# Kernel tuning notes

Measured on AMD Instinct MI355X. Metric: run time of the kernel, lower is better.

## Reference

```python
import jax, jax.numpy as jnp
import numpy as np
import math

B, IN, D, H, DEPTH, E, K = 16384, 128, 512, 8, 3, 8, 2
FF, EH = 4 * D, 256          # ffn width = 4*d_model; expert hidden fixed at 256 in source
EPSILON = 0.1                # forward() default epsilon (exploration mixing)
LN_EPS = 1e-5


def _ln(x, w, b):
    m = x.mean(-1, keepdims=True)
    v = x.var(-1, keepdims=True)  # biased variance, matching nn.LayerNorm
    return (x - m) / jnp.sqrt(v + LN_EPS) * w + b


def setup_inputs() -> dict:
    key = jax.random.key(0)
    ks = jax.random.split(key, 16)
    s = 0.02
    rn = lambda k, shape: jax.random.normal(k, shape, jnp.float32) * s
    return dict(
        x=jax.random.normal(ks[0], (B, IN), jnp.float32),
        embed_w=rn(ks[1], (IN, D)), embed_b=jnp.zeros((D,), jnp.float32),
        ln1_w=jnp.ones((DEPTH, D), jnp.float32), ln1_b=jnp.zeros((DEPTH, D), jnp.float32),
        inproj_w=rn(ks[2], (DEPTH, 3 * D, D)), inproj_b=jnp.zeros((DEPTH, 3 * D), jnp.float32),
        outproj_w=rn(ks[3], (DEPTH, D, D)), outproj_b=jnp.zeros((DEPTH, D), jnp.float32),
        ln2_w=jnp.ones((DEPTH, D), jnp.float32), ln2_b=jnp.zeros((DEPTH, D), jnp.float32),
        ffn_w1=rn(ks[4], (DEPTH, D, FF)), ffn_b1=jnp.zeros((DEPTH, FF), jnp.float32),
        ffn_w2=rn(ks[5], (DEPTH, FF, D)), ffn_b2=jnp.zeros((DEPTH, D), jnp.float32),
        router_w=rn(ks[6], (D, E)), router_b=jnp.zeros((E,), jnp.float32),
        exp_w1=rn(ks[7], (E, D, EH)), exp_b1=jnp.zeros((E, EH), jnp.float32),
        exp_w2=rn(ks[8], (E, EH, D)), exp_b2=jnp.zeros((E, D), jnp.float32),
        head_ln_w=jnp.ones((D,), jnp.float32), head_ln_b=jnp.zeros((D,), jnp.float32),
        head_w=rn(ks[9], (D, 1)), head_b=jnp.zeros((1,), jnp.float32),
    )


def reference(x, embed_w, embed_b, ln1_w, ln1_b, inproj_w, inproj_b,
              outproj_w, outproj_b, ln2_w, ln2_b, ffn_w1, ffn_b1, ffn_w2, ffn_b2,
              router_w, router_b, exp_w1, exp_b1, exp_w2, exp_b2,
              head_ln_w, head_ln_b, head_w, head_b):
    h = x @ embed_w + embed_b                       # [B, D]; unsqueeze(1) -> seq_len == 1
    for l in range(DEPTH):
        g = _ln(h, ln1_w[l], ln1_b[l])
        qkv = g @ inproj_w[l].T + inproj_b[l]       # [B, 3D]
        # seq_len == 1: softmax over the single key is exactly 1, so attn(h,h,h) == out_proj(V)
        v = qkv[:, 2 * D:]
        a = v @ outproj_w[l].T + outproj_b[l]
        h = h + a
        g = _ln(h, ln2_w[l], ln2_b[l])
        h = h + jax.nn.gelu(g @ ffn_w1[l] + ffn_b1[l], approximate=False) @ ffn_w2[l] + ffn_b2[l]
    z = h                                           # squeeze(1)

    # WaggleGate
    logits = z @ router_w + router_b                # [B, E]
    probs = jax.nn.softmax(logits, axis=-1)
    probs = (1.0 - EPSILON) * probs + EPSILON / E
    wts, idx = jax.lax.top_k(probs, K)              # [B, K]
    load = probs.mean(0)
    aux = (load * jnp.log(load * E + 1e-9)).sum() / math.log(E + 1e-9)

    # dense all-expert compute + sparse top-k combine (same math as per-sample dispatch)
    hmid = jax.nn.gelu(jnp.einsum('bd,edh->ebh', z, exp_w1) + exp_b1[:, None, :], approximate=False)
    eo = jnp.einsum('ebh,ehd->ebd', hmid, exp_w2) + exp_b2[:, None, :]   # [E, B, D]
    gate = jnp.zeros((z.shape[0], E), z.dtype).at[
        jnp.arange(z.shape[0])[:, None], idx].add(wts)                    # [B, E]
    moe = jnp.einsum('be,ebd->bd', gate, eo)

    z = z + moe
    logit = (_ln(z, head_ln_w, head_ln_b) @ head_w + head_b)[:, 0]       # [B]
    return logit, aux
```

## Files before the change

kernel.cpp:

```cpp
#include <hip/hip_runtime.h>
#include <hip/hip_bf16.h>

#define B_TOK 16384
#define IN_DIM 128
#define D_DIM 512
#define DEPTH 3
#define NEXP 8
#define FF_DIM 2048
#define EH_DIM 256
#define MAXSLOT 33792
#define MAXTILE 264
#define NHBLK 64

typedef __attribute__((ext_vector_type(8))) __bf16 bf16x8;
typedef __attribute__((ext_vector_type(4))) float f32x4;
typedef __attribute__((ext_vector_type(4))) unsigned short u16x4;
typedef __attribute__((ext_vector_type(8))) unsigned short u16x8;

__device__ __forceinline__ unsigned short f2bf(float f){
    unsigned int u = __float_as_uint(f);
    u += 0x7fffu + ((u >> 16) & 1u);
    return (unsigned short)(u >> 16);
}
__device__ __forceinline__ float bf2f(unsigned short u){
    return __uint_as_float(((unsigned int)u) << 16);
}
__device__ __forceinline__ float geluf(float x){
    return 0.5f * x * (1.0f + erff(x * 0.70710678118654752f));
}
__device__ __forceinline__ void gload_lds16(const void* g, void* l){
    __builtin_amdgcn_global_load_lds((const __attribute__((address_space(1))) unsigned int*)g,
                                     (__attribute__((address_space(3))) unsigned int*)l,
                                     16, 0, 0);
}

__global__ void zero_kernel(int* a, int na, int* b, int nb){
    const int i = blockIdx.x * blockDim.x + threadIdx.x;
    if (i < na) a[i] = 0;
    if (i < nb) b[i] = 0;
}

struct ConvSeg { const float* src; unsigned short* dst; int n4; };
struct ConvArgs { ConvSeg seg[2]; };

__global__ void convert_kernel(ConvArgs a){
    const int stride = gridDim.x * blockDim.x;
    const int tid = blockIdx.x * blockDim.x + threadIdx.x;
    for (int s = 0; s < 2; ++s){
        const f32x4* src = (const f32x4*)a.seg[s].src;
        u16x4* dst = (u16x4*)a.seg[s].dst;
        const int n4 = a.seg[s].n4;
        for (int i = tid; i < n4; i += stride){
            f32x4 v = src[i];
            u16x4 o;
            o[0] = f2bf(v[0]); o[1] = f2bf(v[1]); o[2] = f2bf(v[2]); o[3] = f2bf(v[3]);
            dst[i] = o;
        }
    }
}

struct TSeg { const float* src; unsigned short* dst; int K; int N; int tileStart; };
struct TArgs { TSeg seg[26]; };

__global__ void transpose_kernel(TArgs a){
    __shared__ float t[32][33];
    const int tile = blockIdx.x;
    int s = 0;
    #pragma unroll 1
    while (s < 25 && tile >= a.seg[s+1].tileStart) ++s;
    const TSeg sg = a.seg[s];
    const int local = tile - sg.tileStart;
    const int tilesN = sg.N >> 5;
    const int k0 = (local / tilesN) << 5;
    const int n0 = (local % tilesN) << 5;
    const int tx = threadIdx.x & 31;
    const int ty = threadIdx.x >> 5;
    #pragma unroll
    for (int j = 0; j < 4; ++j)
        t[ty + j*8][tx] = sg.src[(size_t)(k0 + ty + j*8) * sg.N + n0 + tx];
    __syncthreads();
    #pragma unroll
    for (int j = 0; j < 4; ++j){
        const int n = ty + j*8;
        sg.dst[(size_t)(n0 + n) * sg.K + k0 + tx] = f2bf(t[tx][n]);
    }
}

__global__ void foldb_kernel(const float* __restrict__ outproj_w, const float* __restrict__ outproj_b,
                             const float* __restrict__ inproj_b, float* __restrict__ bfold){
    const int l = blockIdx.x, n = threadIdx.x;
    const float* Wo = outproj_w + ((size_t)l*D_DIM + n)*D_DIM;
    const float* bv = inproj_b + l*3*D_DIM + 2*D_DIM;
    float acc = outproj_b[l*D_DIM + n];
    for (int j = 0; j < D_DIM; ++j) acc += Wo[j]*bv[j];
    bfold[l*D_DIM + n] = acc;
}

#define EPI_BF16 0
#define EPI_BF16_GELU 1
#define EPI_F32_BIAS 2
#define EPI_F32_RESID 3

template<int EPI>
__global__ void __launch_bounds__(256, 2)
gemm_bt(const unsigned short* __restrict__ A, const unsigned short* __restrict__ Bt,
        const float* __restrict__ bias, const float* __restrict__ resid,
        void* __restrict__ out, int M, int N, int K)
{
    __shared__ unsigned short sh[16384];
    unsigned short* Al = sh;
    unsigned short* Bl = sh + 8192;
    const int tid  = threadIdx.x;
    const int lane = tid & 63;
    const int wave = tid >> 6;
    const int wm = (wave >> 1) << 6;
    const int wn = (wave & 1) << 6;
    const int bm = blockIdx.y, bn = blockIdx.x;

    f32x4 acc[4][4] = {};

    const unsigned short* Abase = A + (size_t)bm * 128 * K;
    const unsigned short* Bbase = Bt + (size_t)bn * 128 * K;
    const int soff = tid * 16;

    for (int kt = 0; kt < K; kt += 64){
        #pragma unroll
        for (int s = 0; s < 4; ++s){
            const int off = s*4096 + soff;
            const int row = off >> 7, colb = off & 127;
            gload_lds16((const char*)(Abase + (size_t)row*K + kt) + colb, (char*)Al + off);
        }
        #pragma unroll
        for (int s = 0; s < 4; ++s){
            const int off = s*4096 + soff;
            const int row = off >> 7, colb = off & 127;
            gload_lds16((const char*)(Bbase + (size_t)row*K + kt) + colb, (char*)Bl + off);
        }
        __syncthreads();
        #pragma unroll
        for (int ks = 0; ks < 2; ++ks){
            const int k0 = ks*32 + ((lane>>4)<<3);
            bf16x8 af[4], bfr[4];
            #pragma unroll
            for (int i=0;i<4;i++) af[i]  = *(const bf16x8*)&Al[(wm + i*16 + (lane&15))*64 + k0];
            #pragma unroll
            for (int j=0;j<4;j++) bfr[j] = *(const bf16x8*)&Bl[(wn + j*16 + (lane&15))*64 + k0];
            #pragma unroll
            for (int i=0;i<4;i++)
                #pragma unroll
                for (int j=0;j<4;j++)
                    acc[i][j] = __builtin_amdgcn_mfma_f32_16x16x32_bf16(af[i], bfr[j], acc[i][j], 0, 0, 0);
        }
        __syncthreads();
    }

    const int r0 = ((lane>>4)<<2);
    const int cc = lane & 15;

    if (EPI == EPI_F32_BIAS || EPI == EPI_F32_RESID){
        #pragma unroll
        for (int j=0;j<4;j++){
            const int col = bn*128 + wn + j*16 + cc;
            const float bv = bias[col];
            #pragma unroll
            for (int i=0;i<4;i++){
                #pragma unroll
                for (int r=0;r<4;r++){
                    const int row = bm*128 + wm + i*16 + r0 + r;
                    const size_t idx = (size_t)row * N + col;
                    float v = acc[i][j][r] + bv;
                    if (EPI == EPI_F32_BIAS) ((float*)out)[idx] = v;
                    else                     ((float*)out)[idx] = resid[idx] + v;
                }
            }
        }
    } else {
        unsigned short* Ct = sh;
        float bcol[4];
        #pragma unroll
        for (int j=0;j<4;j++) bcol[j] = bias[bn*128 + wn + j*16 + cc];
        #pragma unroll
        for (int i=0;i<4;i++){
            #pragma unroll
            for (int r=0;r<4;r++){
                const int rl = wm + i*16 + r0 + r;
                #pragma unroll
                for (int j=0;j<4;j++){
                    float v = acc[i][j][r] + bcol[j];
                    if (EPI == EPI_BF16_GELU) v = geluf(v);
                    Ct[rl*128 + wn + j*16 + cc] = f2bf(v);
                }
            }
        }
        __syncthreads();
        const int orow = tid >> 4;
        const int ocol = (tid & 15) * 8;
        unsigned short* op = (unsigned short*)out;
        #pragma unroll
        for (int p = 0; p < 8; ++p){
            const int row = p*16 + orow;
            *(u16x4*)(&op[(size_t)(bm*128 + row)*N + bn*128 + ocol])     = *(u16x4*)&Ct[row*128 + ocol];
            *(u16x4*)(&op[(size_t)(bm*128 + row)*N + bn*128 + ocol + 4]) = *(u16x4*)&Ct[row*128 + ocol + 4];
        }
    }
}

#define MEPI_GELU 0
#define MEPI_GATED 1

template<int MEPI, int INDIRECT>
__global__ void __launch_bounds__(256, 2)
gemm_moe(const unsigned short* __restrict__ A, const int* __restrict__ tok,
         const int* __restrict__ offs, const unsigned short* __restrict__ wbase,
         int wstride, const float* __restrict__ bbase, int bstride,
         const float* __restrict__ gslot, unsigned short* __restrict__ out,
         int N, int K)
{
    __shared__ unsigned short sh[16384];
    unsigned short* Al = sh;
    unsigned short* Bl = sh + 8192;
    const int tid  = threadIdx.x;
    const int lane = tid & 63;
    const int wave = tid >> 6;
    const int wm = (wave >> 1) << 6;
    const int wn = (wave & 1) << 6;
    const int bm = blockIdx.y, bn = blockIdx.x;
    const int m0 = bm * 128;
    if (m0 >= offs[8]) return;
    int e = 0;
    #pragma unroll 1
    while (offs[e+1] <= m0) ++e;

    const unsigned short* Bt = wbase + (size_t)e*wstride;
    const float* bias = bbase + (size_t)e*bstride;

    f32x4 acc[4][4] = {};
    const int soff = tid * 16;

    const unsigned short* Arow[4];
    int colb_[4];
    #pragma unroll
    for (int s = 0; s < 4; ++s){
        const int off = s*4096 + soff;
        const int row = off >> 7;
        colb_[s] = off & 127;
        if (INDIRECT){
            const int t = tok[m0 + row];
            Arow[s] = A + (size_t)t*K;
        } else {
            Arow[s] = A + (size_t)(m0 + row)*K;
        }
    }
    const unsigned short* Bbase = Bt + (size_t)bn * 128 * K;

    for (int kt = 0; kt < K; kt += 64){
        #pragma unroll
        for (int s = 0; s < 4; ++s){
            const int off = s*4096 + soff;
            gload_lds16((const char*)(Arow[s] + kt) + colb_[s], (char*)Al + off);
        }
        #pragma unroll
        for (int s = 0; s < 4; ++s){
            const int off = s*4096 + soff;
            const int row = off >> 7, colb = off & 127;
            gload_lds16((const char*)(Bbase + (size_t)row*K + kt) + colb, (char*)Bl + off);
        }
        __syncthreads();
        #pragma unroll
        for (int ks = 0; ks < 2; ++ks){
            const int k0 = ks*32 + ((lane>>4)<<3);
            bf16x8 af[4], bfr[4];
            #pragma unroll
            for (int i=0;i<4;i++) af[i]  = *(const bf16x8*)&Al[(wm + i*16 + (lane&15))*64 + k0];
            #pragma unroll
            for (int j=0;j<4;j++) bfr[j] = *(const bf16x8*)&Bl[(wn + j*16 + (lane&15))*64 + k0];
            #pragma unroll
            for (int i=0;i<4;i++)
                #pragma unroll
                for (int j=0;j<4;j++)
                    acc[i][j] = __builtin_amdgcn_mfma_f32_16x16x32_bf16(af[i], bfr[j], acc[i][j], 0, 0, 0);
        }
        __syncthreads();
    }

    const int r0 = ((lane>>4)<<2);
    const int cc = lane & 15;
    unsigned short* Ct = sh;
    float bcol[4];
    #pragma unroll
    for (int j=0;j<4;j++) bcol[j] = bias[bn*128 + wn + j*16 + cc];
    #pragma unroll
    for (int i=0;i<4;i++){
        #pragma unroll
        for (int r=0;r<4;r++){
            const int rl = wm + i*16 + r0 + r;
            float g = 1.0f;
            if (MEPI == MEPI_GATED) g = gslot[m0 + rl];
            #pragma unroll
            for (int j=0;j<4;j++){
                float v = acc[i][j][r] + bcol[j];
                if (MEPI == MEPI_GELU) v = geluf(v);
                else                   v = v * g;
                Ct[rl*128 + wn + j*16 + cc] = f2bf(v);
            }
        }
    }
    __syncthreads();
    const int orow = tid >> 4;
    const int ocol = (tid & 15) * 8;
    #pragma unroll
    for (int p = 0; p < 8; ++p){
        const int row = p*16 + orow;
        *(u16x4*)(&out[(size_t)(m0 + row)*N + bn*128 + ocol])     = *(u16x4*)&Ct[row*128 + ocol];
        *(u16x4*)(&out[(size_t)(m0 + row)*N + bn*128 + ocol + 4]) = *(u16x4*)&Ct[row*128 + ocol + 4];
    }
}

__global__ void ln_kernel(const float* __restrict__ x, const float* __restrict__ w,
                          const float* __restrict__ b, unsigned short* __restrict__ out)
{
    const int lane = threadIdx.x & 63;
    const int wave = threadIdx.x >> 6;
    const int row  = blockIdx.x * 4 + wave;
    const float* xr = x + (size_t)row * D_DIM;
    f32x4 v0 = *(const f32x4*)(xr + lane*8);
    f32x4 v1 = *(const f32x4*)(xr + lane*8 + 4);
    float s  = v0[0]+v0[1]+v0[2]+v0[3] + v1[0]+v1[1]+v1[2]+v1[3];
    float s2 = v0[0]*v0[0]+v0[1]*v0[1]+v0[2]*v0[2]+v0[3]*v0[3]
             + v1[0]*v1[0]+v1[1]*v1[1]+v1[2]*v1[2]+v1[3]*v1[3];
    #pragma unroll
    for (int o = 32; o > 0; o >>= 1){ s += __shfl_xor(s, o); s2 += __shfl_xor(s2, o); }
    const float mean = s * (1.0f/512.0f);
    const float var  = s2 * (1.0f/512.0f) - mean*mean;
    const float inv  = 1.0f / sqrtf(var + 1e-5f);
    const int k = lane*8;
    u16x4 o0, o1;
    #pragma unroll
    for (int j=0;j<4;j++) o0[j] = f2bf((v0[j]-mean)*inv*w[k+j]   + b[k+j]);
    #pragma unroll
    for (int j=0;j<4;j++) o1[j] = f2bf((v1[j]-mean)*inv*w[k+4+j] + b[k+4+j]);
    *(u16x4*)(out + (size_t)row*D_DIM + k)     = o0;
    *(u16x4*)(out + (size_t)row*D_DIM + k + 4) = o1;
}

__global__ void router_kernel(const float* __restrict__ z, const float* __restrict__ rw,
                              const float* __restrict__ rb, unsigned short* __restrict__ zbf,
                              int2* __restrict__ idx2, float2* __restrict__ wts2,
                              float* __restrict__ bsums)
{
    __shared__ float ps[4][8];
    const int lane = threadIdx.x & 63;
    const int wave = threadIdx.x >> 6;
    const int row  = blockIdx.x * 4 + wave;
    const float* zr = z + (size_t)row * D_DIM;
    f32x4 z0 = *(const f32x4*)(zr + lane*8);
    f32x4 z1 = *(const f32x4*)(zr + lane*8 + 4);
    {
        u16x4 o0, o1;
        #pragma unroll
        for (int j=0;j<4;j++){ o0[j] = f2bf(z0[j]); o1[j] = f2bf(z1[j]); }
        *(u16x4*)(zbf + (size_t)row*D_DIM + lane*8)     = o0;
        *(u16x4*)(zbf + (size_t)row*D_DIM + lane*8 + 4) = o1;
    }
    float acc[8] = {0,0,0,0,0,0,0,0};
    #pragma unroll
    for (int j = 0; j < 8; ++j){
        const float zv = (j < 4) ? z0[j] : z1[j-4];
        const float* wr = rw + (size_t)(lane*8 + j) * 8;
        f32x4 w0 = *(const f32x4*)wr;
        f32x4 w1 = *(const f32x4*)(wr + 4);
        acc[0] += zv*w0[0]; acc[1] += zv*w0[1]; acc[2] += zv*w0[2]; acc[3] += zv*w0[3];
        acc[4] += zv*w1[0]; acc[5] += zv*w1[1]; acc[6] += zv*w1[2]; acc[7] += zv*w1[3];
    }
    #pragma unroll
    for (int o = 32; o > 0; o >>= 1){
        #pragma unroll
        for (int e = 0; e < 8; ++e) acc[e] += __shfl_xor(acc[e], o);
    }
    if (lane == 0){
        float p[8]; float mx = -1e30f;
        #pragma unroll
        for (int e=0;e<8;e++){ p[e] = acc[e] + rb[e]; mx = fmaxf(mx, p[e]); }
        float se = 0.f;
        #pragma unroll
        for (int e=0;e<8;e++){ p[e] = expf(p[e]-mx); se += p[e]; }
        const float sc = 0.9f / se;
        #pragma unroll
        for (int e=0;e<8;e++) p[e] = p[e]*sc + 0.0125f;
        int i1 = 0;
        #pragma unroll
        for (int e=1;e<8;e++) if (p[e] > p[i1]) i1 = e;
        int i2 = (i1 == 0) ? 1 : 0;
        for (int e=i2+1;e<8;e++) if (e != i1 && p[e] > p[i2]) i2 = e;
        idx2[row] = make_int2(i1, i2);
        wts2[row] = make_float2(p[i1], p[i2]);
        #pragma unroll
        for (int e=0;e<8;e++) ps[wave][e] = p[e];
    }
    __syncthreads();
    if (threadIdx.x < 8){
        bsums[blockIdx.x*8 + threadIdx.x] =
            ps[0][threadIdx.x] + ps[1][threadIdx.x] + ps[2][threadIdx.x] + ps[3][threadIdx.x];
    }
}

__global__ void hist_kernel(const int2* __restrict__ idx2, int* __restrict__ blockHist){
    __shared__ int hc[8];
    if (threadIdx.x < 8) hc[threadIdx.x] = 0;
    __syncthreads();
    const int t = blockIdx.x * 256 + threadIdx.x;
    const int2 ii = idx2[t];
    atomicAdd(&hc[ii.x], 1);
    atomicAdd(&hc[ii.y], 1);
    __syncthreads();
    if (threadIdx.x < 8) blockHist[blockIdx.x*8 + threadIdx.x] = hc[threadIdx.x];
}

__global__ void scan_kernel(const int* __restrict__ blockHist, int* __restrict__ offs,
                            int* __restrict__ baseArr){
    if (threadIdx.x == 0){
        int counts[8];
        #pragma unroll
        for (int e=0;e<8;e++) counts[e] = 0;
        for (int b=0;b<NHBLK;b++)
            #pragma unroll
            for (int e=0;e<8;e++) counts[e] += blockHist[b*8+e];
        int o = 0; offs[0] = 0;
        int start[8];
        #pragma unroll
        for (int e=0;e<8;e++){ start[e] = o; o += (counts[e]+127)&~127; offs[e+1] = o; }
        for (int e=0;e<8;e++){
            int cur = start[e];
            for (int b=0;b<NHBLK;b++){ baseArr[b*8+e] = cur; cur += blockHist[b*8+e]; }
        }
    }
}

__global__ void assign_kernel(const int2* __restrict__ idx2, const float2* __restrict__ wts2,
                              const int* __restrict__ baseArr, int2* __restrict__ slot_map,
                              float* __restrict__ gslot, int* __restrict__ tok)
{
    __shared__ int cur[8];
    if (threadIdx.x < 8) cur[threadIdx.x] = 0;
    __syncthreads();
    const int t = blockIdx.x * 256 + threadIdx.x;
    const int2 ii = idx2[t];
    const float2 ww = wts2[t];
    const int r1 = atomicAdd(&cur[ii.x], 1);
    const int r2 = atomicAdd(&cur[ii.y], 1);
    const int s1 = baseArr[blockIdx.x*8 + ii.x] + r1;
    const int s2 = baseArr[blockIdx.x*8 + ii.y] + r2;
    slot_map[t] = make_int2(s1, s2);
    gslot[s1] = ww.x; gslot[s2] = ww.y;
    tok[s1] = t; tok[s2] = t;
}

__global__ void aux_kernel(const float* __restrict__ bsums, float* __restrict__ out_aux)
{
    __shared__ float part[256];
    const int t = threadIdx.x;
    const int e = t & 7, chunk = t >> 3;
    float s = 0.f;
    for (int blk = chunk*128; blk < chunk*128 + 128; ++blk) s += bsums[blk*8 + e];
    part[t] = s;
    __syncthreads();
    if (t < 8){
        float tot = 0.f;
        for (int c = 0; c < 32; ++c) tot += part[c*8 + t];
        part[t] = tot;
    }
    __syncthreads();
    if (t == 0){
        float aux = 0.f;
        for (int e2 = 0; e2 < 8; ++e2){
            float load = part[e2] * (1.0f/16384.0f);
            aux += load * logf(load * 8.0f + 1e-9f);
        }
        out_aux[0] = aux / 2.0794415416798357f;
    }
}

__global__ void head_kernel(const float* __restrict__ h, const unsigned short* __restrict__ eog,
                            const int2* __restrict__ slot_map,
                            const float* __restrict__ w, const float* __restrict__ b,
                            const float* __restrict__ hw, const float* __restrict__ hb,
                            float* __restrict__ out)
{
    const int lane = threadIdx.x & 63;
    const int wave = threadIdx.x >> 6;
    const int row  = blockIdx.x * 4 + wave;
    const int2 sm = slot_map[row];
    const float* zr = h + (size_t)row * D_DIM;
    f32x4 v0 = *(const f32x4*)(zr + lane*8);
    f32x4 v1 = *(const f32x4*)(zr + lane*8 + 4);
    u16x8 e1 = *(const u16x8*)(eog + (size_t)sm.x * D_DIM + lane*8);
    u16x8 e2 = *(const u16x8*)(eog + (size_t)sm.y * D_DIM + lane*8);
    #pragma unroll
    for (int j=0;j<4;j++){ v0[j] += bf2f(e1[j]) + bf2f(e2[j]); }
    #pragma unroll
    for (int j=0;j<4;j++){ v1[j] += bf2f(e1[4+j]) + bf2f(e2[4+j]); }
    float s  = v0[0]+v0[1]+v0[2]+v0[3] + v1[0]+v1[1]+v1[2]+v1[3];
    float s2 = v0[0]*v0[0]+v0[1]*v0[1]+v0[2]*v0[2]+v0[3]*v0[3]
             + v1[0]*v1[0]+v1[1]*v1[1]+v1[2]*v1[2]+v1[3]*v1[3];
    #pragma unroll
    for (int o = 32; o > 0; o >>= 1){ s += __shfl_xor(s, o); s2 += __shfl_xor(s2, o); }
    const float mean = s * (1.0f/512.0f);
    const float var  = s2 * (1.0f/512.0f) - mean*mean;
    const float inv  = 1.0f / sqrtf(var + 1e-5f);
    const int k = lane*8;
    float dot = 0.f;
    #pragma unroll
    for (int j=0;j<4;j++) dot += ((v0[j]-mean)*inv*w[k+j]   + b[k+j])   * hw[k+j];
    #pragma unroll
    for (int j=0;j<4;j++) dot += ((v1[j]-mean)*inv*w[k+4+j] + b[k+4+j]) * hw[k+4+j];
    #pragma unroll
    for (int o = 32; o > 0; o >>= 1) dot += __shfl_xor(dot, o);
    if (lane == 0) out[row] = dot + hb[0];
}

extern "C" void kernel_launch(void* const* d_in, const int* in_sizes, int n_in,
                              void* d_out, int out_size, void* d_ws, size_t ws_size,
                              hipStream_t stream)
{
    (void)in_sizes; (void)n_in; (void)out_size; (void)ws_size;
    const float* x         = (const float*)d_in[0];
    const float* embed_w   = (const float*)d_in[1];
    const float* embed_b   = (const float*)d_in[2];
    const float* ln1_w     = (const float*)d_in[3];
    const float* ln1_b     = (const float*)d_in[4];
    const float* inproj_w  = (const float*)d_in[5];
    const float* inproj_b  = (const float*)d_in[6];
    const float* outproj_w = (const float*)d_in[7];
    const float* outproj_b = (const float*)d_in[8];
    const float* ln2_w     = (const float*)d_in[9];
    const float* ln2_b     = (const float*)d_in[10];
    const float* ffn_w1    = (const float*)d_in[11];
    const float* ffn_b1    = (const float*)d_in[12];
    const float* ffn_w2    = (const float*)d_in[13];
    const float* ffn_b2    = (const float*)d_in[14];
    const float* router_w  = (const float*)d_in[15];
    const float* router_b  = (const float*)d_in[16];
    const float* exp_w1    = (const float*)d_in[17];
    const float* exp_b1    = (const float*)d_in[18];
    const float* exp_w2    = (const float*)d_in[19];
    const float* exp_b2    = (const float*)d_in[20];
    const float* head_ln_w = (const float*)d_in[21];
    const float* head_ln_b = (const float*)d_in[22];
    const float* head_w    = (const float*)d_in[23];
    const float* head_b    = (const float*)d_in[24];

    char* ws = (char*)d_ws;
    unsigned short* xbf   = (unsigned short*)(ws + 0);
    unsigned short* ebf   = (unsigned short*)(ws + 4194304);
    unsigned short* wobf  = (unsigned short*)(ws + 4325376);
    unsigned short* wvtbf = (unsigned short*)(ws + 5898240);
    unsigned short* wfold = (unsigned short*)(ws + 7471104);
    unsigned short* w1t   = (unsigned short*)(ws + 9043968);
    unsigned short* w2t   = (unsigned short*)(ws + 15335424);
    unsigned short* e1t   = (unsigned short*)(ws + 21626880);
    unsigned short* e2t   = (unsigned short*)(ws + 23724032);
    float*          h     = (float*)(ws + 25821184);
    unsigned short* gbf   = (unsigned short*)(ws + 59375616);
    unsigned short* ubf   = (unsigned short*)(ws + 76152832);
    unsigned short* hmidg = ubf;
    unsigned short* eog   = (unsigned short*)(ws + 93454336);
    char* MISC = ws + 143261696;
    int*    offs     = (int*)(MISC + 0);
    float*  zbias    = (float*)(MISC + 256);
    float*  bfold    = (float*)(MISC + 2304);
    int2*   idx2     = (int2*)(MISC + 8448);
    float2* wts2     = (float2*)(MISC + 139520);
    int2*   slot_map = (int2*)(MISC + 270592);
    float*  gslot    = (float*)(MISC + 401664);
    int*    tok      = (int*)(MISC + 536832);
    float*  bsums    = (float*)(MISC + 672000);
    int*    blockHist= (int*)(MISC + 803072);
    int*    baseArr  = (int*)(MISC + 805120);
    unsigned short* zbf = gbf;
    float* out = (float*)d_out;

    zero_kernel<<<(MAXSLOT + 255)/256, 256, 0, stream>>>((int*)zbias, 512, tok, MAXSLOT);

    ConvArgs ca;
    ca.seg[0] = { x, xbf, B_TOK*IN_DIM/4 };
    ca.seg[1] = { outproj_w, wobf, DEPTH*D_DIM*D_DIM/4 };
    convert_kernel<<<1024, 256, 0, stream>>>(ca);

    TArgs ta;
    int tcur = 0, ti = 0;
    ta.seg[ti] = { embed_w, ebf, IN_DIM, D_DIM, tcur };
    tcur += (IN_DIM/32)*(D_DIM/32); ++ti;
    for (int l = 0; l < DEPTH; ++l){
        ta.seg[ti] = { ffn_w1 + (size_t)l*D_DIM*FF_DIM, w1t + (size_t)l*FF_DIM*D_DIM, D_DIM, FF_DIM, tcur };
        tcur += (D_DIM/32)*(FF_DIM/32); ++ti;
    }
    for (int l = 0; l < DEPTH; ++l){
        ta.seg[ti] = { ffn_w2 + (size_t)l*FF_DIM*D_DIM, w2t + (size_t)l*D_DIM*FF_DIM, FF_DIM, D_DIM, tcur };
        tcur += (FF_DIM/32)*(D_DIM/32); ++ti;
    }
    for (int e = 0; e < NEXP; ++e){
        ta.seg[ti] = { exp_w1 + (size_t)e*D_DIM*EH_DIM, e1t + (size_t)e*EH_DIM*D_DIM, D_DIM, EH_DIM, tcur };
        tcur += (D_DIM/32)*(EH_DIM/32); ++ti;
    }
    for (int e = 0; e < NEXP; ++e){
        ta.seg[ti] = { exp_w2 + (size_t)e*EH_DIM*D_DIM, e2t + (size_t)e*D_DIM*EH_DIM, EH_DIM, D_DIM, tcur };
        tcur += (EH_DIM/32)*(D_DIM/32); ++ti;
    }
    for (int l = 0; l < DEPTH; ++l){
        ta.seg[ti] = { inproj_w + (size_t)l*3*D_DIM*D_DIM + 2*D_DIM*D_DIM,
                       wvtbf + (size_t)l*D_DIM*D_DIM, D_DIM, D_DIM, tcur };
        tcur += (D_DIM/32)*(D_DIM/32); ++ti;
    }
    transpose_kernel<<<tcur, 256, 0, stream>>>(ta);

    foldb_kernel<<<DEPTH, D_DIM, 0, stream>>>(outproj_w, outproj_b, inproj_b, bfold);

    const dim3 blk(256);
    for (int l = 0; l < DEPTH; ++l){
        gemm_bt<EPI_BF16><<<dim3(4, 4), blk, 0, stream>>>(
            wobf + (size_t)l*D_DIM*D_DIM, wvtbf + (size_t)l*D_DIM*D_DIM,
            zbias, nullptr, wfold + (size_t)l*D_DIM*D_DIM, D_DIM, D_DIM, D_DIM);
    }

    gemm_bt<EPI_F32_BIAS><<<dim3(D_DIM/128, B_TOK/128), blk, 0, stream>>>(
        xbf, ebf, embed_b, nullptr, h, B_TOK, D_DIM, IN_DIM);

    for (int l = 0; l < DEPTH; ++l){
        ln_kernel<<<B_TOK/4, 256, 0, stream>>>(h, ln1_w + l*D_DIM, ln1_b + l*D_DIM, gbf);
        gemm_bt<EPI_F32_RESID><<<dim3(D_DIM/128, B_TOK/128), blk, 0, stream>>>(
            gbf, wfold + (size_t)l*D_DIM*D_DIM, bfold + l*D_DIM, h, h, B_TOK, D_DIM, D_DIM);
        ln_kernel<<<B_TOK/4, 256, 0, stream>>>(h, ln2_w + l*D_DIM, ln2_b + l*D_DIM, gbf);
        gemm_bt<EPI_BF16_GELU><<<dim3(FF_DIM/128, B_TOK/128), blk, 0, stream>>>(
            gbf, w1t + (size_t)l*FF_DIM*D_DIM, ffn_b1 + l*FF_DIM, nullptr, ubf, B_TOK, FF_DIM, D_DIM);
        gemm_bt<EPI_F32_RESID><<<dim3(D_DIM/128, B_TOK/128), blk, 0, stream>>>(
            ubf, w2t + (size_t)l*D_DIM*FF_DIM, ffn_b2 + l*D_DIM, h, h, B_TOK, D_DIM, FF_DIM);
    }

    router_kernel<<<B_TOK/4, 256, 0, stream>>>(h, router_w, router_b, zbf, idx2, wts2, bsums);
    aux_kernel<<<1, 256, 0, stream>>>(bsums, out + B_TOK);
    hist_kernel<<<NHBLK, 256, 0, stream>>>(idx2, blockHist);
    scan_kernel<<<1, 64, 0, stream>>>(blockHist, offs, baseArr);
    assign_kernel<<<NHBLK, 256, 0, stream>>>(idx2, wts2, baseArr, slot_map, gslot, tok);

    gemm_moe<MEPI_GELU, 1><<<dim3(EH_DIM/128, MAXTILE), blk, 0, stream>>>(
        zbf, tok, offs, e1t, EH_DIM*D_DIM, exp_b1, EH_DIM, nullptr, hmidg, EH_DIM, D_DIM);
    gemm_moe<MEPI_GATED, 0><<<dim3(D_DIM/128, MAXTILE), blk, 0, stream>>>(
        hmidg, nullptr, offs, e2t, D_DIM*EH_DIM, exp_b2, D_DIM, gslot, eog, D_DIM, EH_DIM);

    head_kernel<<<B_TOK/4, 256, 0, stream>>>(h, eog, slot_map, head_ln_w, head_ln_b, head_w, head_b, out);
}
```

Baseline: 705.5 us.

## Double-buffer LDS staging in GEMMs and add XCD-aware 1D block swizzle

Both GEMM kernels now use two LDS buffers (64KB) so the global-to-LDS load of the next K tile is issued before the MFMA compute on the current tile, dropping one barrier per iteration. Launches switch to a 1D grid that is remapped so consecutive logical tiles land on the same XCD, which is meant to improve L2 reuse of the shared A/B panels. The larger LDS footprint may limit occupancy to two blocks per CU. The M dimension parameter is replaced by the tile count along N.

```diff
diff --git a/kernel.cpp b/kernel.cpp
--- a/kernel.cpp
+++ b/kernel.cpp
@@ -32,6 +32,12 @@
     __builtin_amdgcn_global_load_lds((const __attribute__((address_space(1))) unsigned int*)g,
                                      (__attribute__((address_space(3))) unsigned int*)l,
                                      16, 0, 0);
+}
+__device__ __forceinline__ int xcd_swizzle(int orig, int nwg){
+    const int q = nwg >> 3, r = nwg & 7;
+    const int xcd = orig & 7;
+    const int idx = orig >> 3;
+    return (xcd < r ? xcd*(q+1) : r*(q+1) + (xcd-r)*q) + idx;
 }
 
 __global__ void zero_kernel(int* a, int na, int* b, int nb){
@@ -105,17 +111,19 @@
 __global__ void __launch_bounds__(256, 2)
 gemm_bt(const unsigned short* __restrict__ A, const unsigned short* __restrict__ Bt,
         const float* __restrict__ bias, const float* __restrict__ resid,
-        void* __restrict__ out, int M, int N, int K)
-{
-    __shared__ unsigned short sh[16384];
-    unsigned short* Al = sh;
-    unsigned short* Bl = sh + 8192;
+        void* __restrict__ out, int NB, int N, int K)
+{
+    __shared__ unsigned short sh[32768];
+    const int nwg = gridDim.x;
+    const int wg  = xcd_swizzle(blockIdx.x, nwg);
+    const int bn  = wg % NB;
+    const int bm  = wg / NB;
+
     const int tid  = threadIdx.x;
     const int lane = tid & 63;
     const int wave = tid >> 6;
     const int wm = (wave >> 1) << 6;
     const int wn = (wave & 1) << 6;
-    const int bm = blockIdx.y, bn = blockIdx.x;
 
     f32x4 acc[4][4] = {};
 
@@ -123,35 +131,50 @@
     const unsigned short* Bbase = Bt + (size_t)bn * 128 * K;
     const int soff = tid * 16;
 
-    for (int kt = 0; kt < K; kt += 64){
+    auto STAGE = [&](int b, int kt){
+        char* Ab = (char*)(sh + b*16384);
+        char* Bb = (char*)(sh + b*16384 + 8192);
         #pragma unroll
         for (int s = 0; s < 4; ++s){
             const int off = s*4096 + soff;
             const int row = off >> 7, colb = off & 127;
-            gload_lds16((const char*)(Abase + (size_t)row*K + kt) + colb, (char*)Al + off);
+            gload_lds16((const char*)(Abase + (size_t)row*K + kt) + colb, Ab + off);
         }
         #pragma unroll
         for (int s = 0; s < 4; ++s){
             const int off = s*4096 + soff;
             const int row = off >> 7, colb = off & 127;
-            gload_lds16((const char*)(Bbase + (size_t)row*K + kt) + colb, (char*)Bl + off);
-        }
-        __syncthreads();
+            gload_lds16((const char*)(Bbase + (size_t)row*K + kt) + colb, Bb + off);
+        }
+    };
+    auto COMPUTE = [&](int b){
+        const unsigned short* Ab = sh + b*16384;
+        const unsigned short* Bb = sh + b*16384 + 8192;
         #pragma unroll
         for (int ks = 0; ks < 2; ++ks){
             const int k0 = ks*32 + ((lane>>4)<<3);
             bf16x8 af[4], bfr[4];
             #pragma unroll
-            for (int i=0;i<4;i++) af[i]  = *(const bf16x8*)&Al[(wm + i*16 + (lane&15))*64 + k0];
-            #pragma unroll
-            for (int j=0;j<4;j++) bfr[j] = *(const bf16x8*)&Bl[(wn + j*16 + (lane&15))*64 + k0];
+            for (int i=0;i<4;i++) af[i]  = *(const bf16x8*)&Ab[(wm + i*16 + (lane&15))*64 + k0];
+            #pragma unroll
+            for (int j=0;j<4;j++) bfr[j] = *(const bf16x8*)&Bb[(wn + j*16 + (lane&15))*64 + k0];
             #pragma unroll
             for (int i=0;i<4;i++)
                 #pragma unroll
                 for (int j=0;j<4;j++)
                     acc[i][j] = __builtin_amdgcn_mfma_f32_16x16x32_bf16(af[i], bfr[j], acc[i][j], 0, 0, 0);
         }
+    };
+
+    STAGE(0, 0);
+    __syncthreads();
+    const int nk = K >> 6;
+    int cur = 0;
+    for (int i = 0; i < nk; ++i){
+        if (i + 1 < nk) STAGE(cur ^ 1, (i + 1) << 6);
+        COMPUTE(cur);
         __syncthreads();
+        cur ^= 1;
     }
 
     const int r0 = ((lane>>4)<<2);
@@ -214,19 +237,22 @@
          const int* __restrict__ offs, const unsigned short* __restrict__ wbase,
          int wstride, const float* __restrict__ bbase, int bstride,
          const float* __restrict__ gslot, unsigned short* __restrict__ out,
-         int N, int K)
-{
-    __shared__ unsigned short sh[16384];
-    unsigned short* Al = sh;
-    unsigned short* Bl = sh + 8192;
+         int NB, int N, int K)
+{
+    __shared__ unsigned short sh[32768];
+    const int nwg = gridDim.x;
+    const int wg  = xcd_swizzle(blockIdx.x, nwg);
+    const int bn  = wg % NB;
+    const int bm  = wg / NB;
+    const int m0  = bm * 128;
+    if (m0 >= offs[8]) return;
+
     const int tid  = threadIdx.x;
     const int lane = tid & 63;
     const int wave = tid >> 6;
     const int wm = (wave >> 1) << 6;
     const int wn = (wave & 1) << 6;
-    const int bm = blockIdx.y, bn = blockIdx.x;
-    const int m0 = bm * 128;
-    if (m0 >= offs[8]) return;
+
     int e = 0;
     #pragma unroll 1
     while (offs[e+1] <= m0) ++e;
@@ -253,34 +279,49 @@
     }
     const unsigned short* Bbase = Bt + (size_t)bn * 128 * K;
 
-    for (int kt = 0; kt < K; kt += 64){
+    auto STAGE = [&](int b, int kt){
+        char* Ab = (char*)(sh + b*16384);
+        char* Bb = (char*)(sh + b*16384 + 8192);
         #pragma unroll
         for (int s = 0; s < 4; ++s){
             const int off = s*4096 + soff;
-            gload_lds16((const char*)(Arow[s] + kt) + colb_[s], (char*)Al + off);
+            gload_lds16((const char*)(Arow[s] + kt) + colb_[s], Ab + off);
         }
         #pragma unroll
         for (int s = 0; s < 4; ++s){
             const int off = s*4096 + soff;
             const int row = off >> 7, colb = off & 127;
-            gload_lds16((const char*)(Bbase + (size_t)row*K + kt) + colb, (char*)Bl + off);
-        }
-        __syncthreads();
+            gload_lds16((const char*)(Bbase + (size_t)row*K + kt) + colb, Bb + off);
+        }
+    };
+    auto COMPUTE = [&](int b){
+        const unsigned short* Ab = sh + b*16384;
+        const unsigned short* Bb = sh + b*16384 + 8192;
         #pragma unroll
         for (int ks = 0; ks < 2; ++ks){
             const int k0 = ks*32 + ((lane>>4)<<3);
             bf16x8 af[4], bfr[4];
             #pragma unroll
-            for (int i=0;i<4;i++) af[i]  = *(const bf16x8*)&Al[(wm + i*16 + (lane&15))*64 + k0];
-            #pragma unroll
-            for (int j=0;j<4;j++) bfr[j] = *(const bf16x8*)&Bl[(wn + j*16 + (lane&15))*64 + k0];
+            for (int i=0;i<4;i++) af[i]  = *(const bf16x8*)&Ab[(wm + i*16 + (lane&15))*64 + k0];
+            #pragma unroll
+            for (int j=0;j<4;j++) bfr[j] = *(const bf16x8*)&Bb[(wn + j*16 + (lane&15))*64 + k0];
             #pragma unroll
             for (int i=0;i<4;i++)
                 #pragma unroll
                 for (int j=0;j<4;j++)
                     acc[i][j] = __builtin_amdgcn_mfma_f32_16x16x32_bf16(af[i], bfr[j], acc[i][j], 0, 0, 0);
         }
+    };
+
+    STAGE(0, 0);
+    __syncthreads();
+    const int nk = K >> 6;
+    int cur = 0;
+    for (int i = 0; i < nk; ++i){
+        if (i + 1 < nk) STAGE(cur ^ 1, (i + 1) << 6);
+        COMPUTE(cur);
         __syncthreads();
+        cur ^= 1;
     }
 
     const int r0 = ((lane>>4)<<2);
@@ -617,23 +658,23 @@
 
     const dim3 blk(256);
     for (int l = 0; l < DEPTH; ++l){
-        gemm_bt<EPI_BF16><<<dim3(4, 4), blk, 0, stream>>>(
+        gemm_bt<EPI_BF16><<<16, blk, 0, stream>>>(
             wobf + (size_t)l*D_DIM*D_DIM, wvtbf + (size_t)l*D_DIM*D_DIM,
-            zbias, nullptr, wfold + (size_t)l*D_DIM*D_DIM, D_DIM, D_DIM, D_DIM);
-    }
-
-    gemm_bt<EPI_F32_BIAS><<<dim3(D_DIM/128, B_TOK/128), blk, 0, stream>>>(
-        xbf, ebf, embed_b, nullptr, h, B_TOK, D_DIM, IN_DIM);
+            zbias, nullptr, wfold + (size_t)l*D_DIM*D_DIM, 4, D_DIM, D_DIM);
+    }
+
+    gemm_bt<EPI_F32_BIAS><<<(D_DIM/128)*(B_TOK/128), blk, 0, stream>>>(
+        xbf, ebf, embed_b, nullptr, h, D_DIM/128, D_DIM, IN_DIM);
 
     for (int l = 0; l < DEPTH; ++l){
         ln_kernel<<<B_TOK/4, 256, 0, stream>>>(h, ln1_w + l*D_DIM, ln1_b + l*D_DIM, gbf);
-        gemm_bt<EPI_F32_RESID><<<dim3(D_DIM/128, B_TOK/128), blk, 0, stream>>>(
-            gbf, wfold + (size_t)l*D_DIM*D_DIM, bfold + l*D_DIM, h, h, B_TOK, D_DIM, D_DIM);
+        gemm_bt<EPI_F32_RESID><<<(D_DIM/128)*(B_TOK/128), blk, 0, stream>>>(
+            gbf, wfold + (size_t)l*D_DIM*D_DIM, bfold + l*D_DIM, h, h, D_DIM/128, D_DIM, D_DIM);
         ln_kernel<<<B_TOK/4, 256, 0, stream>>>(h, ln2_w + l*D_DIM, ln2_b + l*D_DIM, gbf);
-        gemm_bt<EPI_BF16_GELU><<<dim3(FF_DIM/128, B_TOK/128), blk, 0, stream>>>(
-            gbf, w1t + (size_t)l*FF_DIM*D_DIM, ffn_b1 + l*FF_DIM, nullptr, ubf, B_TOK, FF_DIM, D_DIM);
-        gemm_bt<EPI_F32_RESID><<<dim3(D_DIM/128, B_TOK/128), blk, 0, stream>>>(
-            ubf, w2t + (size_t)l*D_DIM*FF_DIM, ffn_b2 + l*D_DIM, h, h, B_TOK, D_DIM, FF_DIM);
+        gemm_bt<EPI_BF16_GELU><<<(FF_DIM/128)*(B_TOK/128), blk, 0, stream>>>(
+            gbf, w1t + (size_t)l*FF_DIM*D_DIM, ffn_b1 + l*FF_DIM, nullptr, ubf, FF_DIM/128, FF_DIM, D_DIM);
+        gemm_bt<EPI_F32_RESID><<<(D_DIM/128)*(B_TOK/128), blk, 0, stream>>>(
+            ubf, w2t + (size_t)l*D_DIM*FF_DIM, ffn_b2 + l*D_DIM, h, h, D_DIM/128, D_DIM, FF_DIM);
     }
 
     router_kernel<<<B_TOK/4, 256, 0, stream>>>(h, router_w, router_b, zbf, idx2, wts2, bsums);
@@ -642,10 +683,10 @@
     scan_kernel<<<1, 64, 0, stream>>>(blockHist, offs, baseArr);
     assign_kernel<<<NHBLK, 256, 0, stream>>>(idx2, wts2, baseArr, slot_map, gslot, tok);
 
-    gemm_moe<MEPI_GELU, 1><<<dim3(EH_DIM/128, MAXTILE), blk, 0, stream>>>(
-        zbf, tok, offs, e1t, EH_DIM*D_DIM, exp_b1, EH_DIM, nullptr, hmidg, EH_DIM, D_DIM);
-    gemm_moe<MEPI_GATED, 0><<<dim3(D_DIM/128, MAXTILE), blk, 0, stream>>>(
-        hmidg, nullptr, offs, e2t, D_DIM*EH_DIM, exp_b2, D_DIM, gslot, eog, D_DIM, EH_DIM);
+    gemm_moe<MEPI_GELU, 1><<<(EH_DIM/128)*MAXTILE, blk, 0, stream>>>(
+        zbf, tok, offs, e1t, EH_DIM*D_DIM, exp_b1, EH_DIM, nullptr, hmidg, EH_DIM/128, EH_DIM, D_DIM);
+    gemm_moe<MEPI_GATED, 0><<<(D_DIM/128)*MAXTILE, blk, 0, stream>>>(
+        hmidg, nullptr, offs, e2t, D_DIM*EH_DIM, exp_b2, D_DIM, gslot, eog, D_DIM/128, D_DIM, EH_DIM);
 
     head_kernel<<<B_TOK/4, 256, 0, stream>>>(h, eog, slot_map, head_ln_w, head_ln_b, head_w, head_b, out);
 }
```

Measured after the change: 697.5 us. About the same (-1.1%).
